# Kernel optimization log

Hardware: AMD Instinct MI355X
Metric: run time of the kernel (lower is better)

Reference implementation:

```python
import jax, jax.numpy as jnp
import numpy as np

B, T, I, H = 256, 1024, 128, 256


def setup_inputs() -> dict:
    key = jax.random.key(0)
    ks = jax.random.split(key, 10)
    p = lambda k, shape: jax.random.normal(k, shape, dtype=jnp.float32) * 0.1
    return {
        "x": jax.random.normal(ks[0], (B, T, I), dtype=jnp.float32),
        # forget gate
        "f_wh": p(ks[1], (H, H)), "f_wx": p(ks[2], (I, H)), "f_b": p(ks[3], (H,)),
        # input (create) gate: potential (tanh) and percent (sigmoid) branches
        "i_wh_pot": p(ks[4], (H, H)), "i_wx_pot": p(ks[5], (I, H)), "i_b_pot": p(ks[6], (H,)),
        "i_wh_perc": p(ks[7], (H, H)), "i_wx_perc": p(ks[8], (I, H)), "i_b_perc": p(ks[9], (H,)),
        # output gate
        "o_wh": p(jax.random.fold_in(key, 10), (H, H)),
        "o_wx": p(jax.random.fold_in(key, 11), (I, H)),
        "o_b": p(jax.random.fold_in(key, 12), (H,)),
    }


def reference(x, f_wh, f_wx, f_b, i_wh_pot, i_wx_pot, i_b_pot,
              i_wh_perc, i_wx_perc, i_b_perc, o_wh, o_wx, o_b):
    # x: [B, T, I]
    sigmoid, tanh = jax.nn.sigmoid, jnp.tanh

    def step(carry, xt):  # xt: [B, I]
        s, l = carry  # short_term [B,H], long_term [B,H]
        forget = sigmoid(s @ f_wh + xt @ f_wx + f_b)
        create = sigmoid(s @ i_wh_perc + xt @ i_wx_perc + i_b_perc) * \
                 tanh(s @ i_wh_pot + xt @ i_wx_pot + i_b_pot)
        l_new = forget * l + create
        s_new = tanh(l_new) * sigmoid(s @ o_wh + xt @ o_wx + o_b)
        return (s_new, l_new), None

    init = (jnp.zeros((x.shape[0], f_b.shape[0]), x.dtype),
            jnp.zeros((x.shape[0], f_b.shape[0]), x.dtype))
    (short_term, long_term), _ = jax.lax.scan(step, init, jnp.swapaxes(x, 0, 1))
    return short_term, long_term
```

## Files before the change

kernel.cpp:

```cpp
#include <hip/hip_runtime.h>
#include <cstdint>

#define T_STEPS 1024
#define I_DIM 128
#define H_DIM 256

typedef __attribute__((ext_vector_type(8))) short bf16x8;
typedef __attribute__((ext_vector_type(4))) float f32x4;
typedef __attribute__((ext_vector_type(2))) unsigned int u32x2;

__device__ __forceinline__ uint32_t f2bf(float f) {
    uint32_t u = __builtin_bit_cast(uint32_t, f);
    return (u + 0x7FFFu + ((u >> 16) & 1u)) >> 16;
}
__device__ __forceinline__ uint32_t pk2bf(float lo, float hi) {
    return (f2bf(lo) & 0xFFFFu) | (f2bf(hi) << 16);
}
__device__ __forceinline__ float sigmoid_(float v) { return 1.f / (1.f + __expf(-v)); }
__device__ __forceinline__ float tanh_(float v) { float e = __expf(2.f * v); return 1.f - 2.f / (e + 1.f); }

__device__ __forceinline__ void barrier_lgkm() {
    asm volatile("s_waitcnt lgkmcnt(0)\n\ts_barrier" ::: "memory");
}

__global__ void __launch_bounds__(256, 1)
lstm_kernel(const float* __restrict__ x,
            const float* __restrict__ f_wh, const float* __restrict__ f_wx, const float* __restrict__ f_b,
            const float* __restrict__ p_wh, const float* __restrict__ p_wx, const float* __restrict__ p_b,
            const float* __restrict__ c_wh, const float* __restrict__ c_wx, const float* __restrict__ c_b,
            const float* __restrict__ o_wh, const float* __restrict__ o_wx, const float* __restrict__ o_b,
            float* __restrict__ out, uint8_t* __restrict__ ws)
{
    __shared__ __align__(16) uint8_t lds[65792];
    uint8_t* WH = lds;
    uint8_t* WX = lds + 32768;
    uint8_t* SL = lds + 49152;
    uint8_t* XT = lds + 57344;
    float*   GB = (float*)(lds + 61440);

    const int tid  = (int)threadIdx.x;
    const int lane = tid & 63;
    const int wv   = tid >> 6;
    const int blk  = (int)blockIdx.x;
    const int grp  = blk & 15;
    const int cwg  = blk >> 4;
    const int grow0 = grp << 4;
    const int hc0   = cwg << 4;

    uint8_t* sbase = ws + 4096;

    const float* wh = (wv == 0) ? f_wh : (wv == 1) ? p_wh : (wv == 2) ? c_wh : o_wh;
    const float* wx = (wv == 0) ? f_wx : (wv == 1) ? p_wx : (wv == 2) ? c_wx : o_wx;
    const float* bp = (wv == 0) ? f_b  : (wv == 1) ? p_b  : (wv == 2) ? c_b  : o_b;

    {
        const int col = lane & 15, kc = lane >> 4;
        const uint32_t csw = (uint32_t)((col & 7) << 4);
        uint8_t* whb = WH + (size_t)(wv * 16 + col) * 512;
        #pragma unroll
        for (int it = 0; it < 8; ++it) {
            const int k0 = it * 32 + kc * 8;
            float v0 = wh[(size_t)(k0 + 0) * H_DIM + hc0 + col];
            float v1 = wh[(size_t)(k0 + 1) * H_DIM + hc0 + col];
            float v2 = wh[(size_t)(k0 + 2) * H_DIM + hc0 + col];
            float v3 = wh[(size_t)(k0 + 3) * H_DIM + hc0 + col];
            float v4 = wh[(size_t)(k0 + 4) * H_DIM + hc0 + col];
            float v5 = wh[(size_t)(k0 + 5) * H_DIM + hc0 + col];
            float v6 = wh[(size_t)(k0 + 6) * H_DIM + hc0 + col];
            float v7 = wh[(size_t)(k0 + 7) * H_DIM + hc0 + col];
            uint4 pk;
            pk.x = pk2bf(v0, v1); pk.y = pk2bf(v2, v3);
            pk.z = pk2bf(v4, v5); pk.w = pk2bf(v6, v7);
            *(uint4*)(whb + (((uint32_t)(it * 64 + kc * 16)) ^ csw)) = pk;
        }
        uint8_t* wxb = WX + (size_t)(wv * 16 + col) * 256;
        #pragma unroll
        for (int it = 0; it < 4; ++it) {
            const int k0 = it * 32 + kc * 8;
            float v0 = wx[(size_t)(k0 + 0) * H_DIM + hc0 + col];
            float v1 = wx[(size_t)(k0 + 1) * H_DIM + hc0 + col];
            float v2 = wx[(size_t)(k0 + 2) * H_DIM + hc0 + col];
            float v3 = wx[(size_t)(k0 + 3) * H_DIM + hc0 + col];
            float v4 = wx[(size_t)(k0 + 4) * H_DIM + hc0 + col];
            float v5 = wx[(size_t)(k0 + 5) * H_DIM + hc0 + col];
            float v6 = wx[(size_t)(k0 + 6) * H_DIM + hc0 + col];
            float v7 = wx[(size_t)(k0 + 7) * H_DIM + hc0 + col];
            uint4 pk;
            pk.x = pk2bf(v0, v1); pk.y = pk2bf(v2, v3);
            pk.z = pk2bf(v4, v5); pk.w = pk2bf(v6, v7);
            *(uint4*)(wxb + (((uint32_t)(it * 64 + kc * 16)) ^ csw)) = pk;
        }
    }
    const float bias = bp[hc0 + (lane & 15)];
    __syncthreads();

    const int fr = lane & 15, fkc = lane >> 4;
    const uint32_t fsw = (uint32_t)((fr & 7) << 4);
    uint8_t* slA = SL + (size_t)fr * 512;
    uint8_t* xtA = XT + (size_t)fr * 256;
    const uint8_t* whB = WH + (size_t)(wv * 16 + fr) * 512;
    const uint8_t* wxB = WX + (size_t)(wv * 16 + fr) * 256;

    uint4 bwh[8], bwx[4];
    #pragma unroll
    for (int q = 0; q < 8; ++q)
        bwh[q] = *(const uint4*)(whB + (((uint32_t)(q * 64 + fkc * 16)) ^ fsw));
    #pragma unroll
    for (int q = 0; q < 4; ++q)
        bwx[q] = *(const uint4*)(wxB + (((uint32_t)(q * 64 + fkc * 16)) ^ fsw));

    const int crow = tid >> 4, ccol = tid & 15;

    if ((tid & 1) == 0) {
        uint8_t* pdst = sbase + (size_t)(grow0 + crow) * 1024 + (size_t)(cwg * 8 + (ccol >> 1)) * 8;
        u32x2 pd; pd.x = 0u; pd.y = 1u;
        asm volatile("global_atomic_swap_x2 %0, %1, off sc1" :: "v"(pdst), "v"(pd) : "memory");
    }

    const int xrow = tid >> 4, xseg = tid & 15;
    const uint32_t xsw = (uint32_t)((xrow & 7) << 4);
    const float* xptr = x + (size_t)(grow0 + xrow) * (T_STEPS * I_DIM) + xseg * 8;
    float4 xr0 = *(const float4*)(xptr);
    float4 xr1 = *(const float4*)(xptr + 4);

    float l_reg = 0.f, s_fin = 0.f, l_fin = 0.f;

    for (int t = 0; t < T_STEPS; ++t) {
        {
            uint4 pk;
            pk.x = pk2bf(xr0.x, xr0.y); pk.y = pk2bf(xr0.z, xr0.w);
            pk.z = pk2bf(xr1.x, xr1.y); pk.w = pk2bf(xr1.z, xr1.w);
            *(uint4*)(XT + (size_t)xrow * 256 + (((uint32_t)(xseg * 16)) ^ xsw)) = pk;
        }
        {
            const int tn = (t + 1 < T_STEPS) ? (t + 1) : (T_STEPS - 1);
            const float* p = xptr + (size_t)tn * I_DIM;
            xr0 = *(const float4*)(p);
            xr1 = *(const float4*)(p + 4);
        }
        barrier_lgkm();

        f32x4 accA = {0.f, 0.f, 0.f, 0.f};
        #pragma unroll
        for (int q = 0; q < 4; ++q) {
            uint4 av = *(const uint4*)(xtA + (((uint32_t)(q * 64 + fkc * 16)) ^ fsw));
            accA = __builtin_amdgcn_mfma_f32_16x16x32_bf16(
                __builtin_bit_cast(bf16x8, av), __builtin_bit_cast(bf16x8, bwx[q]), accA, 0, 0, 0);
        }

        uint4 g0, g1, g2, g3;
        const uint32_t e = (uint32_t)t + 1u;
        const uint8_t* src = sbase + (size_t)((t & 1) ? 262144 : 0)
                           + (size_t)(grow0 + xrow) * 1024 + (size_t)xseg * 64;
        for (;;) {
            asm volatile("global_load_dwordx4 %0, %1, off sc0 sc1"
                         : "=v"(g0) : "v"(src) : "memory");
            asm volatile("global_load_dwordx4 %0, %1, off offset:16 sc0 sc1"
                         : "=v"(g1) : "v"(src) : "memory");
            asm volatile("global_load_dwordx4 %0, %1, off offset:32 sc0 sc1"
                         : "=v"(g2) : "v"(src) : "memory");
            asm volatile("global_load_dwordx4 %0, %1, off offset:48 sc0 sc1"
                         : "=v"(g3) : "v"(src) : "memory");
            asm volatile("s_waitcnt vmcnt(0)" ::: "memory");
            __builtin_amdgcn_sched_barrier(0);
            const uint32_t m = (g0.y ^ e) | (g0.w ^ e) | (g1.y ^ e) | (g1.w ^ e)
                             | (g2.y ^ e) | (g2.w ^ e) | (g3.y ^ e) | (g3.w ^ e);
            if (m == 0) break;
            asm volatile("s_sleep 1");
        }

        {
            uint4 d0; d0.x = g0.x; d0.y = g0.z; d0.z = g1.x; d0.w = g1.z;
            uint4 d1; d1.x = g2.x; d1.y = g2.z; d1.z = g3.x; d1.w = g3.z;
            uint8_t* dst = SL + (size_t)xrow * 512;
            const uint32_t o = (uint32_t)(xseg * 32);
            *(uint4*)(dst + (o ^ xsw)) = d0;
            *(uint4*)(dst + ((o + 16) ^ xsw)) = d1;
        }
        barrier_lgkm();

        f32x4 accB = {0.f, 0.f, 0.f, 0.f};
        #pragma unroll
        for (int q = 0; q < 4; ++q) {
            uint4 a0 = *(const uint4*)(slA + (((uint32_t)(q * 64 + fkc * 16)) ^ fsw));
            uint4 a1 = *(const uint4*)(slA + (((uint32_t)((q + 4) * 64 + fkc * 16)) ^ fsw));
            accA = __builtin_amdgcn_mfma_f32_16x16x32_bf16(
                __builtin_bit_cast(bf16x8, a0), __builtin_bit_cast(bf16x8, bwh[q]), accA, 0, 0, 0);
            accB = __builtin_amdgcn_mfma_f32_16x16x32_bf16(
                __builtin_bit_cast(bf16x8, a1), __builtin_bit_cast(bf16x8, bwh[q + 4]), accB, 0, 0, 0);
        }

        #pragma unroll
        for (int j = 0; j < 4; ++j) {
            const float pre = accA[j] + accB[j] + bias;
            const float a = (wv == 1) ? tanh_(pre) : sigmoid_(pre);
            GB[wv * 272 + (fkc * 4 + j) * 17 + fr] = a;
        }
        barrier_lgkm();

        {
            const float fg  = GB[0 * 272 + crow * 17 + ccol];
            const float pot = GB[1 * 272 + crow * 17 + ccol];
            const float prc = GB[2 * 272 + crow * 17 + ccol];
            const float og  = GB[3 * 272 + crow * 17 + ccol];
            const float lnew = fg * l_reg + prc * pot;
            const float snew = tanh_(lnew) * og;
            l_reg = lnew;
            if (t == T_STEPS - 1) { s_fin = snew; l_fin = lnew; }
            const uint32_t sb = f2bf(snew);
            const uint32_t ob = (uint32_t)__shfl_xor((int)sb, 1, 64);
            if (((tid & 1) == 0) && (t != T_STEPS - 1)) {
                uint8_t* pdst = sbase + (size_t)(((t + 1) & 1) ? 262144 : 0)
                              + (size_t)(grow0 + crow) * 1024 + (size_t)(cwg * 8 + (ccol >> 1)) * 8;
                u32x2 pd; pd.x = (sb & 0xFFFFu) | (ob << 16); pd.y = (uint32_t)t + 2u;
                asm volatile("global_atomic_swap_x2 %0, %1, off sc1" :: "v"(pdst), "v"(pd) : "memory");
            }
        }
    }

    out[(size_t)(grow0 + crow) * H_DIM + hc0 + ccol] = s_fin;
    out[(size_t)H_DIM * H_DIM + (size_t)(grow0 + crow) * H_DIM + hc0 + ccol] = l_fin;
}

extern "C" void kernel_launch(void* const* d_in, const int* in_sizes, int n_in,
                              void* d_out, int out_size, void* d_ws, size_t ws_size,
                              hipStream_t stream) {
    const float* x    = (const float*)d_in[0];
    const float* f_wh = (const float*)d_in[1];
    const float* f_wx = (const float*)d_in[2];
    const float* f_b  = (const float*)d_in[3];
    const float* p_wh = (const float*)d_in[4];
    const float* p_wx = (const float*)d_in[5];
    const float* p_b  = (const float*)d_in[6];
    const float* c_wh = (const float*)d_in[7];
    const float* c_wx = (const float*)d_in[8];
    const float* c_b  = (const float*)d_in[9];
    const float* o_wh = (const float*)d_in[10];
    const float* o_wx = (const float*)d_in[11];
    const float* o_b  = (const float*)d_in[12];
    float* outp = (float*)d_out;
    uint8_t* wsp = (uint8_t*)d_ws;

    hipMemsetAsync(d_ws, 0, 4096 + 2 * 262144, stream);

    void* args[] = { (void*)&x,
                     (void*)&f_wh, (void*)&f_wx, (void*)&f_b,
                     (void*)&p_wh, (void*)&p_wx, (void*)&p_b,
                     (void*)&c_wh, (void*)&c_wx, (void*)&c_b,
                     (void*)&o_wh, (void*)&o_wx, (void*)&o_b,
                     (void*)&outp, (void*)&wsp };
    hipLaunchCooperativeKernel((const void*)lstm_kernel, dim3(256), dim3(256), args, 0, stream);
}
```

Measured before the change: 2.000 ms.

## Add fast non-coherent polling path with coherent mirror fallback for state exchange

Each hidden-state publish is now written twice: a plain store to a fast buffer and a system-coherent store to a mirror buffer. This replaces the atomic swap. Consumers first poll the fast buffer with sc0-only loads, which are cheaper, for a bounded number of rounds. If the data never shows up there, they switch permanently to polling the mirror with sc0 sc1 loads. The aim is to cut cross-workgroup handoff latency per timestep, at the cost of twice the stores, a larger workspace, and a possible stall of the budgeted rounds if the fast path never sees the data.

```diff
diff --git a/kernel.cpp b/kernel.cpp
--- a/kernel.cpp
+++ b/kernel.cpp
@@ -47,7 +47,8 @@
     const int grow0 = grp << 4;
     const int hc0   = cwg << 4;
 
-    uint8_t* sbase = ws + 4096;
+    uint8_t* FAST = ws + 4096;
+    uint8_t* MIRR = ws + 4096 + 524288;
 
     const float* wh = (wv == 0) ? f_wh : (wv == 1) ? p_wh : (wv == 2) ? c_wh : o_wh;
     const float* wx = (wv == 0) ? f_wx : (wv == 1) ? p_wx : (wv == 2) ? c_wx : o_wx;
@@ -110,11 +111,12 @@
         bwx[q] = *(const uint4*)(wxB + (((uint32_t)(q * 64 + fkc * 16)) ^ fsw));
 
     const int crow = tid >> 4, ccol = tid & 15;
+    const size_t pub_off = (size_t)(grow0 + crow) * 1024 + (size_t)(cwg * 8 + (ccol >> 1)) * 8;
 
     if ((tid & 1) == 0) {
-        uint8_t* pdst = sbase + (size_t)(grow0 + crow) * 1024 + (size_t)(cwg * 8 + (ccol >> 1)) * 8;
         u32x2 pd; pd.x = 0u; pd.y = 1u;
-        asm volatile("global_atomic_swap_x2 %0, %1, off sc1" :: "v"(pdst), "v"(pd) : "memory");
+        asm volatile("global_store_dwordx2 %0, %1, off" :: "v"(FAST + pub_off), "v"(pd) : "memory");
+        asm volatile("global_store_dwordx2 %0, %1, off sc0 sc1" :: "v"(MIRR + pub_off), "v"(pd) : "memory");
     }
 
     const int xrow = tid >> 4, xseg = tid & 15;
@@ -123,6 +125,9 @@
     float4 xr0 = *(const float4*)(xptr);
     float4 xr1 = *(const float4*)(xptr + 4);
 
+    const size_t poll_off = (size_t)(grow0 + xrow) * 1024 + (size_t)xseg * 64;
+
+    bool slow = false;
     float l_reg = 0.f, s_fin = 0.f, l_fin = 0.f;
 
     for (int t = 0; t < T_STEPS; ++t) {
@@ -149,24 +154,46 @@
         }
 
         uint4 g0, g1, g2, g3;
+        uint32_t m = 1u;
         const uint32_t e = (uint32_t)t + 1u;
-        const uint8_t* src = sbase + (size_t)((t & 1) ? 262144 : 0)
-                           + (size_t)(grow0 + xrow) * 1024 + (size_t)xseg * 64;
-        for (;;) {
-            asm volatile("global_load_dwordx4 %0, %1, off sc0 sc1"
-                         : "=v"(g0) : "v"(src) : "memory");
-            asm volatile("global_load_dwordx4 %0, %1, off offset:16 sc0 sc1"
-                         : "=v"(g1) : "v"(src) : "memory");
-            asm volatile("global_load_dwordx4 %0, %1, off offset:32 sc0 sc1"
-                         : "=v"(g2) : "v"(src) : "memory");
-            asm volatile("global_load_dwordx4 %0, %1, off offset:48 sc0 sc1"
-                         : "=v"(g3) : "v"(src) : "memory");
-            asm volatile("s_waitcnt vmcnt(0)" ::: "memory");
-            __builtin_amdgcn_sched_barrier(0);
-            const uint32_t m = (g0.y ^ e) | (g0.w ^ e) | (g1.y ^ e) | (g1.w ^ e)
-                             | (g2.y ^ e) | (g2.w ^ e) | (g3.y ^ e) | (g3.w ^ e);
-            if (m == 0) break;
-            asm volatile("s_sleep 1");
+        const size_t par = (size_t)((t & 1) ? 262144 : 0);
+        if (!slow) {
+            const uint8_t* src = FAST + par + poll_off;
+            const int budget = (t == 0) ? 1024 : 64;
+            int rounds = 0;
+            do {
+                asm volatile("global_load_dwordx4 %0, %1, off sc0"
+                             : "=v"(g0) : "v"(src) : "memory");
+                asm volatile("global_load_dwordx4 %0, %1, off offset:16 sc0"
+                             : "=v"(g1) : "v"(src) : "memory");
+                asm volatile("global_load_dwordx4 %0, %1, off offset:32 sc0"
+                             : "=v"(g2) : "v"(src) : "memory");
+                asm volatile("global_load_dwordx4 %0, %1, off offset:48 sc0"
+                             : "=v"(g3) : "v"(src) : "memory");
+                asm volatile("s_waitcnt vmcnt(0)" ::: "memory");
+                __builtin_amdgcn_sched_barrier(0);
+                m = (g0.y ^ e) | (g0.w ^ e) | (g1.y ^ e) | (g1.w ^ e)
+                  | (g2.y ^ e) | (g2.w ^ e) | (g3.y ^ e) | (g3.w ^ e);
+                if (m == 0) break;
+            } while (++rounds < budget);
+            if (m != 0) slow = true;
+        }
+        if (m != 0) {
+            const uint8_t* src = MIRR + par + poll_off;
+            do {
+                asm volatile("global_load_dwordx4 %0, %1, off sc0 sc1"
+                             : "=v"(g0) : "v"(src) : "memory");
+                asm volatile("global_load_dwordx4 %0, %1, off offset:16 sc0 sc1"
+                             : "=v"(g1) : "v"(src) : "memory");
+                asm volatile("global_load_dwordx4 %0, %1, off offset:32 sc0 sc1"
+                             : "=v"(g2) : "v"(src) : "memory");
+                asm volatile("global_load_dwordx4 %0, %1, off offset:48 sc0 sc1"
+                             : "=v"(g3) : "v"(src) : "memory");
+                asm volatile("s_waitcnt vmcnt(0)" ::: "memory");
+                __builtin_amdgcn_sched_barrier(0);
+                m = (g0.y ^ e) | (g0.w ^ e) | (g1.y ^ e) | (g1.w ^ e)
+                  | (g2.y ^ e) | (g2.w ^ e) | (g3.y ^ e) | (g3.w ^ e);
+            } while (m != 0);
         }
 
         {
@@ -210,10 +237,10 @@
             const uint32_t sb = f2bf(snew);
             const uint32_t ob = (uint32_t)__shfl_xor((int)sb, 1, 64);
             if (((tid & 1) == 0) && (t != T_STEPS - 1)) {
-                uint8_t* pdst = sbase + (size_t)(((t + 1) & 1) ? 262144 : 0)
-                              + (size_t)(grow0 + crow) * 1024 + (size_t)(cwg * 8 + (ccol >> 1)) * 8;
+                const size_t po = (size_t)(((t + 1) & 1) ? 262144 : 0) + pub_off;
                 u32x2 pd; pd.x = (sb & 0xFFFFu) | (ob << 16); pd.y = (uint32_t)t + 2u;
-                asm volatile("global_atomic_swap_x2 %0, %1, off sc1" :: "v"(pdst), "v"(pd) : "memory");
+                asm volatile("global_store_dwordx2 %0, %1, off" :: "v"(FAST + po), "v"(pd) : "memory");
+                asm volatile("global_store_dwordx2 %0, %1, off sc0 sc1" :: "v"(MIRR + po), "v"(pd) : "memory");
             }
         }
     }
@@ -241,7 +268,7 @@
     float* outp = (float*)d_out;
     uint8_t* wsp = (uint8_t*)d_ws;
 
-    hipMemsetAsync(d_ws, 0, 4096 + 2 * 262144, stream);
+    hipMemsetAsync(d_ws, 0, 4096 + 2 * 524288, stream);
 
     void* args[] = { (void*)&x,
                      (void*)&f_wh, (void*)&f_wx, (void*)&f_b,
```

Result: slower. 2.431 ms (+21.5%).

## Use per-workgroup ready flags and plain stores for cross-block state exchange

Applied to the files above, without the earlier changes.

Each workgroup now publishes its recurrent state with plain system-scope stores instead of atomic swaps. After a barrier, one thread writes a per-workgroup step counter into a small flag array. Consumers spin on that flag word first, then issue the state loads before the x-projection MFMAs so the fetch overlaps compute. The existing tag check stays as a fallback retry loop. This aims to cut polling traffic and atomic cost on the serial critical path, at the price of an extra flag round trip and an extra barrier per step, and it relies on the ordering between the data stores and the flag store.

```diff
diff --git a/kernel.cpp b/kernel.cpp
--- a/kernel.cpp
+++ b/kernel.cpp
@@ -110,11 +110,17 @@
         bwx[q] = *(const uint4*)(wxB + (((uint32_t)(q * 64 + fkc * 16)) ^ fsw));
 
     const int crow = tid >> 4, ccol = tid & 15;
+    const size_t pub_off = (size_t)(grow0 + crow) * 1024 + (size_t)(cwg * 8 + (ccol >> 1)) * 8;
 
     if ((tid & 1) == 0) {
-        uint8_t* pdst = sbase + (size_t)(grow0 + crow) * 1024 + (size_t)(cwg * 8 + (ccol >> 1)) * 8;
         u32x2 pd; pd.x = 0u; pd.y = 1u;
-        asm volatile("global_atomic_swap_x2 %0, %1, off sc1" :: "v"(pdst), "v"(pd) : "memory");
+        asm volatile("global_store_dwordx2 %0, %1, off sc0 sc1" :: "v"(sbase + pub_off), "v"(pd) : "memory");
+    }
+    asm volatile("s_barrier" ::: "memory");
+    if (tid == 0) {
+        const uint32_t h = 1u;
+        asm volatile("global_store_dword %0, %1, off sc0 sc1"
+                     :: "v"(ws + (size_t)grp * 64 + (size_t)cwg * 4), "v"(h) : "memory");
     }
 
     const int xrow = tid >> 4, xseg = tid & 15;
@@ -123,6 +129,9 @@
     float4 xr0 = *(const float4*)(xptr);
     float4 xr1 = *(const float4*)(xptr + 4);
 
+    const size_t poll_off = (size_t)(grow0 + xrow) * 1024 + (size_t)xseg * 64;
+    const uint8_t* hintp = ws + (size_t)grp * 64 + (size_t)xseg * 4;
+
     float l_reg = 0.f, s_fin = 0.f, l_fin = 0.f;
 
     for (int t = 0; t < T_STEPS; ++t) {
@@ -140,6 +149,26 @@
         }
         barrier_lgkm();
 
+        const uint32_t e = (uint32_t)t + 1u;
+        {
+            uint32_t h;
+            for (;;) {
+                asm volatile("global_load_dword %0, %1, off sc0 sc1"
+                             : "=v"(h) : "v"(hintp) : "memory");
+                asm volatile("s_waitcnt vmcnt(0)" ::: "memory");
+                __builtin_amdgcn_sched_barrier(0);
+                if (__all(h >= e)) break;
+            }
+        }
+
+        uint4 g0, g1, g2, g3;
+        const size_t par = (size_t)((t & 1) ? 262144 : 0);
+        const uint8_t* src = sbase + par + poll_off;
+        asm volatile("global_load_dwordx4 %0, %1, off sc0 sc1" : "=v"(g0) : "v"(src) : "memory");
+        asm volatile("global_load_dwordx4 %0, %1, off offset:16 sc0 sc1" : "=v"(g1) : "v"(src) : "memory");
+        asm volatile("global_load_dwordx4 %0, %1, off offset:32 sc0 sc1" : "=v"(g2) : "v"(src) : "memory");
+        asm volatile("global_load_dwordx4 %0, %1, off offset:48 sc0 sc1" : "=v"(g3) : "v"(src) : "memory");
+
         f32x4 accA = {0.f, 0.f, 0.f, 0.f};
         #pragma unroll
         for (int q = 0; q < 4; ++q) {
@@ -148,25 +177,21 @@
                 __builtin_bit_cast(bf16x8, av), __builtin_bit_cast(bf16x8, bwx[q]), accA, 0, 0, 0);
         }
 
-        uint4 g0, g1, g2, g3;
-        const uint32_t e = (uint32_t)t + 1u;
-        const uint8_t* src = sbase + (size_t)((t & 1) ? 262144 : 0)
-                           + (size_t)(grow0 + xrow) * 1024 + (size_t)xseg * 64;
-        for (;;) {
-            asm volatile("global_load_dwordx4 %0, %1, off sc0 sc1"
-                         : "=v"(g0) : "v"(src) : "memory");
-            asm volatile("global_load_dwordx4 %0, %1, off offset:16 sc0 sc1"
-                         : "=v"(g1) : "v"(src) : "memory");
-            asm volatile("global_load_dwordx4 %0, %1, off offset:32 sc0 sc1"
-                         : "=v"(g2) : "v"(src) : "memory");
-            asm volatile("global_load_dwordx4 %0, %1, off offset:48 sc0 sc1"
-                         : "=v"(g3) : "v"(src) : "memory");
-            asm volatile("s_waitcnt vmcnt(0)" ::: "memory");
-            __builtin_amdgcn_sched_barrier(0);
-            const uint32_t m = (g0.y ^ e) | (g0.w ^ e) | (g1.y ^ e) | (g1.w ^ e)
-                             | (g2.y ^ e) | (g2.w ^ e) | (g3.y ^ e) | (g3.w ^ e);
-            if (m == 0) break;
-            asm volatile("s_sleep 1");
+        asm volatile("s_waitcnt vmcnt(0)" ::: "memory");
+        __builtin_amdgcn_sched_barrier(0);
+        {
+            uint32_t m = (g0.y ^ e) | (g0.w ^ e) | (g1.y ^ e) | (g1.w ^ e)
+                       | (g2.y ^ e) | (g2.w ^ e) | (g3.y ^ e) | (g3.w ^ e);
+            while (m != 0) {
+                asm volatile("global_load_dwordx4 %0, %1, off sc0 sc1" : "=v"(g0) : "v"(src) : "memory");
+                asm volatile("global_load_dwordx4 %0, %1, off offset:16 sc0 sc1" : "=v"(g1) : "v"(src) : "memory");
+                asm volatile("global_load_dwordx4 %0, %1, off offset:32 sc0 sc1" : "=v"(g2) : "v"(src) : "memory");
+                asm volatile("global_load_dwordx4 %0, %1, off offset:48 sc0 sc1" : "=v"(g3) : "v"(src) : "memory");
+                asm volatile("s_waitcnt vmcnt(0)" ::: "memory");
+                __builtin_amdgcn_sched_barrier(0);
+                m = (g0.y ^ e) | (g0.w ^ e) | (g1.y ^ e) | (g1.w ^ e)
+                  | (g2.y ^ e) | (g2.w ^ e) | (g3.y ^ e) | (g3.w ^ e);
+            }
         }
 
         {
@@ -210,10 +235,17 @@
             const uint32_t sb = f2bf(snew);
             const uint32_t ob = (uint32_t)__shfl_xor((int)sb, 1, 64);
             if (((tid & 1) == 0) && (t != T_STEPS - 1)) {
-                uint8_t* pdst = sbase + (size_t)(((t + 1) & 1) ? 262144 : 0)
-                              + (size_t)(grow0 + crow) * 1024 + (size_t)(cwg * 8 + (ccol >> 1)) * 8;
+                const size_t po = (size_t)(((t + 1) & 1) ? 262144 : 0) + pub_off;
                 u32x2 pd; pd.x = (sb & 0xFFFFu) | (ob << 16); pd.y = (uint32_t)t + 2u;
-                asm volatile("global_atomic_swap_x2 %0, %1, off sc1" :: "v"(pdst), "v"(pd) : "memory");
+                asm volatile("global_store_dwordx2 %0, %1, off sc0 sc1" :: "v"(sbase + po), "v"(pd) : "memory");
+            }
+        }
+        if (t != T_STEPS - 1) {
+            asm volatile("s_barrier" ::: "memory");
+            if (tid == 0) {
+                const uint32_t h = (uint32_t)t + 2u;
+                asm volatile("global_store_dword %0, %1, off sc0 sc1"
+                             :: "v"(ws + (size_t)grp * 64 + (size_t)cwg * 4), "v"(h) : "memory");
             }
         }
     }
```

Result: slower. 2.410 ms (+20.5%).
